# Kernel tuning notes

Hardware: AMD Instinct MI355X
Metric: run time of the kernel (lower is better)

The kernel has to match this reference:

```python
import jax, jax.numpy as jnp
import numpy as np

NU = 160000   # users
NM = 60000    # movies
D = 64        # embedding dim
E = 5000000   # rating edges
L = 200000    # label edges to score
NUM_LAYERS = 3


def setup_inputs() -> dict:
    key = jax.random.key(0)
    k1, k2, k3, k4, k5, k6 = jax.random.split(key, 6)
    return {
        "emb_user": jax.random.normal(k1, (NU, D), jnp.float32),
        "emb_movie": jax.random.normal(k2, (NM, D), jnp.float32),
        "node_id_user": jnp.arange(NU),
        "node_id_movie": jnp.arange(NM),
        "edge_from": jax.random.randint(k3, (E,), 0, NM),   # movie side of each edge
        "edge_to": jax.random.randint(k4, (E,), 0, NU),     # user side of each edge
        "label_movie": jax.random.randint(k5, (L,), 0, NM),
        "label_user": jax.random.randint(k6, (L,), 0, NU),
    }


def reference(emb_user, emb_movie, node_id_user, node_id_movie,
              edge_from, edge_to, label_movie, label_user):
    # Embedding lookup (node_id is an arange over all nodes in the batch)
    x_u = emb_user[node_id_user]    # [NU, D]
    x_m = emb_movie[node_id_movie]  # [NM, D]

    # Symmetric degree normalization: deg(from)^-1/2 * deg(to)^-1/2 per edge
    ones = jnp.ones(edge_from.shape[0], dtype=x_m.dtype)
    deg_m = jax.ops.segment_sum(ones, edge_from, num_segments=NM)
    deg_u = jax.ops.segment_sum(ones, edge_to, num_segments=NU)
    inv_m = jnp.where(deg_m > 0, deg_m ** -0.5, 0.0)
    inv_u = jnp.where(deg_u > 0, deg_u ** -0.5, 0.0)
    norm = inv_m[edge_from] * inv_u[edge_to]  # [E]

    # NOTE: the original torch code never writes the propagated embeddings back
    # into x_dict, so every layer propagates the layer-0 embeddings. Replicated
    # faithfully here.
    embs_u = [x_u]
    embs_m = [x_m]
    for _ in range(NUM_LAYERS):
        # movie -> user aggregation (x2y): gather movie feats, scale, scatter-add to users
        u_agg = jax.ops.segment_sum(norm[:, None] * x_m[edge_from], edge_to, num_segments=NU)
        m_agg = jax.ops.segment_sum(norm[:, None] * x_u[edge_to], edge_from, num_segments=NM)
        embs_u.append(u_agg)
        embs_m.append(m_agg)

    # Layer combination with weights 1/(l+1)
    w = 1.0 / (jnp.arange(NUM_LAYERS + 1, dtype=x_u.dtype) + 1.0)
    res_u = jnp.einsum('l,lnd->nd', w, jnp.stack(embs_u))  # [NU, D]
    res_m = jnp.einsum('l,lnd->nd', w, jnp.stack(embs_m))  # [NM, D]

    # Classifier: dot product over label edges
    scores = jnp.sum(res_u[label_user] * res_m[label_movie], axis=-1)  # [L]
    return (scores, res_u, res_m)
```

## Files before the change

kernel.cpp:

```cpp
#include <hip/hip_runtime.h>
#include <hip/hip_bf16.h>

#define NU 160000
#define NM 60000
#define DD 64
#define NE 5000000
#define NL 200000

#define COEF (13.0f / 12.0f)

#define SHIFT_U 9
#define SHIFT_M 7
#define NBU ((NU + (1 << SHIFT_U) - 1) >> SHIFT_U)
#define NBM ((NM + (1 << SHIFT_M) - 1) >> SHIFT_M)
#define VB_U 16
#define VB_M 18

#define UDIV 30000
#define LG_U 1
#define MDIV 20000
#define BS 1024
#define NVU2 (NBU << 10)
#define NVM2 (NBM << 10)


#define CEC 16

__global__ void bucket_count_kernel(const int* __restrict__ ef, const int* __restrict__ et,
                                    int* __restrict__ gbh_u, int* __restrict__ gbh_m) {
    __shared__ int bhu[NBU], bhm[NBM];
    int tid = threadIdx.x;
    for (int i = tid; i < NBU; i += 256) bhu[i] = 0;
    for (int i = tid; i < NBM; i += 256) bhm[i] = 0;
    __syncthreads();
    int base = (blockIdx.x * 256 + tid) * CEC;
    if (base < NE) {
        const int4* f4 = (const int4*)(ef + base);
        const int4* t4 = (const int4*)(et + base);
        #pragma unroll
        for (int q = 0; q < CEC / 4; q++) {
            int4 ff = f4[q]; int4 tt = t4[q];
            atomicAdd(&bhm[ff.x >> SHIFT_M], 1); atomicAdd(&bhu[tt.x >> SHIFT_U], 1);
            atomicAdd(&bhm[ff.y >> SHIFT_M], 1); atomicAdd(&bhu[tt.y >> SHIFT_U], 1);
            atomicAdd(&bhm[ff.z >> SHIFT_M], 1); atomicAdd(&bhu[tt.z >> SHIFT_U], 1);
            atomicAdd(&bhm[ff.w >> SHIFT_M], 1); atomicAdd(&bhu[tt.w >> SHIFT_U], 1);
        }
    }
    __syncthreads();
    for (int i = tid; i < NBU; i += 256) if (bhu[i]) atomicAdd(&gbh_u[i], bhu[i]);
    for (int i = tid; i < NBM; i += 256) if (bhm[i]) atomicAdd(&gbh_m[i], bhm[i]);
}


__global__ void scan_small_kernel(const int* __restrict__ in, int* __restrict__ out,
                                  int* __restrict__ cur, int n) {
    __shared__ int buf[256];
    int tid = threadIdx.x;
    int idx = tid * 4;
    int v0 = (idx + 0 < n) ? in[idx + 0] : 0;
    int v1 = (idx + 1 < n) ? in[idx + 1] : 0;
    int v2 = (idx + 2 < n) ? in[idx + 2] : 0;
    int v3 = (idx + 3 < n) ? in[idx + 3] : 0;
    int s = v0 + v1 + v2 + v3;
    buf[tid] = s;
    __syncthreads();
    for (int off = 1; off < 256; off <<= 1) {
        int t = (tid >= off) ? buf[tid - off] : 0;
        __syncthreads();
        buf[tid] += t;
        __syncthreads();
    }
    int p = buf[tid] - s;
    if (idx + 0 < n) { out[idx + 0] = p; if (cur) cur[idx + 0] = p; p += v0; }
    if (idx + 1 < n) { out[idx + 1] = p; if (cur) cur[idx + 1] = p; p += v1; }
    if (idx + 2 < n) { out[idx + 2] = p; if (cur) cur[idx + 2] = p; p += v2; }
    if (idx + 3 < n) { out[idx + 3] = p; if (cur) cur[idx + 3] = p; p += v3; }
    if (tid == 255) out[n] = buf[255];
}


#define PEC 16

__global__ void partition_kernel(const int* __restrict__ key, const int* __restrict__ val,
                                 int* __restrict__ bcur, int* __restrict__ stage,
                                 int nb, int shift, int valbits, int mode) {
    __shared__ int lh[512];
    __shared__ int lbase[512];
    int tid = threadIdx.x;
    for (int i = tid; i < nb; i += 256) lh[i] = 0;
    __syncthreads();
    int base = (blockIdx.x * 256 + tid) * PEC;
    int lk_[PEC], v_[PEC], br_[PEC];
    bool act = base < NE;
    if (act) {
        int k_[PEC];
        const int4* k4 = (const int4*)(key + base);
        const int4* v4 = (const int4*)(val + base);
        #pragma unroll
        for (int q = 0; q < PEC / 4; q++) {
            int4 kk = k4[q]; int4 vv = v4[q];
            k_[q * 4 + 0] = kk.x; k_[q * 4 + 1] = kk.y; k_[q * 4 + 2] = kk.z; k_[q * 4 + 3] = kk.w;
            v_[q * 4 + 0] = vv.x; v_[q * 4 + 1] = vv.y; v_[q * 4 + 2] = vv.z; v_[q * 4 + 3] = vv.w;
        }
        #pragma unroll
        for (int q = 0; q < PEC; q++) {
            int k = k_[q];
            int lk;
            if (mode == 0) lk = ((k & 511) << 1) | (v_[q] >= UDIV ? 1 : 0);
            else           lk = ((int)((unsigned)v_[q] / MDIV) << 7) | (k & 127);
            lk_[q] = lk;
            int b = k >> shift;
            int r = atomicAdd(&lh[b], 1);
            br_[q] = (b << 13) | r;
        }
    }
    __syncthreads();
    for (int i = tid; i < nb; i += 256) lbase[i] = lh[i] ? atomicAdd(&bcur[i], lh[i]) : 0;
    __syncthreads();
    if (act) {
        #pragma unroll
        for (int q = 0; q < PEC; q++) {
            int b = br_[q] >> 13;
            int r = br_[q] & 8191;
            stage[lbase[b] + r] = (lk_[q] << valbits) | v_[q];
        }
    }
}


__global__ void build_kernel(const int* __restrict__ stage, const int* __restrict__ bo,
                             int* __restrict__ rp, int* __restrict__ pay,
                             int n, int valbits, int pmask) {
    __shared__ int cnt[BS];
    __shared__ int tmp[BS];
    int b = blockIdx.x;
    int tid = threadIdx.x;
    int base = b << 10;
    int nn = min(BS, n - base);
    int vmask = (1 << valbits) - 1;
    int s0 = bo[b];
    int s1 = bo[b + 1];

    for (int i = tid; i < BS; i += 256) cnt[i] = 0;
    __syncthreads();
    for (int e = s0 + tid; e < s1; e += 256)
        atomicAdd(&cnt[stage[e] >> valbits], 1);
    __syncthreads();
    int ov[4];
    #pragma unroll
    for (int q = 0; q < 4; q++) ov[q] = cnt[tid + q * 256];
    for (int off = 1; off < BS; off <<= 1) {
        int t[4];
        #pragma unroll
        for (int q = 0; q < 4; q++) {
            int i = tid + q * 256;
            t[q] = (i >= off) ? cnt[i - off] : 0;
        }
        __syncthreads();
        #pragma unroll
        for (int q = 0; q < 4; q++) cnt[tid + q * 256] += t[q];
        __syncthreads();
    }
    #pragma unroll
    for (int q = 0; q < 4; q++) {
        int i = tid + q * 256;
        int excl = cnt[i] - ov[q];
        tmp[i] = s0 + excl;
        if (i < nn) rp[base + i] = s0 + excl;
    }
    if (b == 0 && tid == 0) rp[n] = NE;
    __syncthreads();
    for (int e = s0 + tid; e < s1; e += 256) {
        int p = stage[e];
        int k = p >> valbits;
        int pos = atomicAdd(&tmp[k], 1);
        pay[pos] = (p & vmask) | ((k & pmask) << valbits);
    }
}


__global__ void inv_from_rp_kernel(const int* __restrict__ rp, float* __restrict__ inv,
                                   int n, int lg) {
    int i = blockIdx.x * blockDim.x + threadIdx.x;
    if (i < n) {
        int d = rp[(i + 1) << lg] - rp[i << lg];
        inv[i] = (d > 0) ? rsqrtf((float)d) : 0.0f;
    }
}

__global__ void inv_m_from_rp_kernel(const int* __restrict__ rp, float* __restrict__ inv) {
    int f = blockIdx.x * blockDim.x + threadIdx.x;
    if (f < NM) {
        int base = ((f >> 7) << 10) | (f & 127);
        int d = 0;
        #pragma unroll
        for (int h = 0; h < 8; h++) {
            int idx = base + (h << 7);
            d += rp[idx + 1] - rp[idx];
        }
        inv[f] = (d > 0) ? rsqrtf((float)d) : 0.0f;
    }
}


__global__ void prescale_kernel(const float* __restrict__ x, const float* __restrict__ inv,
                                __hip_bfloat16* __restrict__ y, int total) {
    int i = blockIdx.x * blockDim.x + threadIdx.x;
    if (i < total) {
        int node = i >> 6;
        y[i] = __float2bfloat16(inv[node] * x[i]);
    }
}


__global__ void gather_u_kernel(const int* __restrict__ rp, const int* __restrict__ pay,
                                const float* __restrict__ inv_dst,
                                const __hip_bfloat16* __restrict__ y_src,
                                const float* __restrict__ x_dst,
                                float* __restrict__ res, int n) {
    int tid = blockIdx.x * blockDim.x + threadIdx.x;
    int node = tid >> 6;
    int lane = threadIdx.x & 63;
    if (node >= n) return;
    int start = rp[node << LG_U];
    int end   = rp[(node + 1) << LG_U];
    float acc = 0.0f;
    for (int i = start; i < end; i += 64) {
        int cnt = min(end - i, 64);
        int nid = (lane < cnt) ? pay[i + lane] : 0;
        int j = 0;
        for (; j + 4 <= cnt; j += 4) {
            int f0 = __shfl(nid, j + 0, 64);
            int f1 = __shfl(nid, j + 1, 64);
            int f2 = __shfl(nid, j + 2, 64);
            int f3 = __shfl(nid, j + 3, 64);
            float a0 = __bfloat162float(y_src[f0 * DD + lane]);
            float a1 = __bfloat162float(y_src[f1 * DD + lane]);
            float a2 = __bfloat162float(y_src[f2 * DD + lane]);
            float a3 = __bfloat162float(y_src[f3 * DD + lane]);
            acc += a0 + a1 + a2 + a3;
        }
        for (; j < cnt; j++) {
            int f0 = __shfl(nid, j, 64);
            acc += __bfloat162float(y_src[f0 * DD + lane]);
        }
    }
    int o = node * DD + lane;
    res[o] = x_dst[o] + COEF * inv_dst[node] * acc;
}


__global__ __launch_bounds__(1024) void gather_m_kernel(
        const int* __restrict__ rp, const int* __restrict__ pay,
        const float* __restrict__ inv_dst,
        const __hip_bfloat16* __restrict__ y_src,
        const float* __restrict__ x_dst,
        float* __restrict__ res) {
    __shared__ float acc[128 * DD];
    int b = blockIdx.x;
    int tid = threadIdx.x;
    int wave = tid >> 6;
    int lane = tid & 63;
    for (int i = tid; i < 128 * DD; i += 1024) acc[i] = 0.0f;
    __syncthreads();

    int vbase = b << 10;
    const int umask = (1 << VB_M) - 1;
    float racc = 0.0f;
    int rm = -1;
    for (int h = 0; h < 8; h++) {
        int s0 = rp[vbase + (h << 7)];
        int s1 = rp[vbase + (h << 7) + 128];
        int total = s1 - s0;
        if (total <= 0) continue;
        int per = (total + 15) >> 4;
        int e0 = s0 + wave * per;
        int e1 = min(e0 + per, s1);
        for (int i = e0; i < e1; i += 64) {
            int cnt = min(e1 - i, 64);
            int pv = (lane < cnt) ? pay[i + lane] : 0;
            int j = 0;
            for (; j + 4 <= cnt; j += 4) {
                int p0 = __shfl(pv, j + 0, 64);
                int p1 = __shfl(pv, j + 1, 64);
                int p2 = __shfl(pv, j + 2, 64);
                int p3 = __shfl(pv, j + 3, 64);
                float a0 = __bfloat162float(y_src[(p0 & umask) * DD + lane]);
                float a1 = __bfloat162float(y_src[(p1 & umask) * DD + lane]);
                float a2 = __bfloat162float(y_src[(p2 & umask) * DD + lane]);
                float a3 = __bfloat162float(y_src[(p3 & umask) * DD + lane]);
                int m0 = p0 >> VB_M;
                if (m0 != rm) { if (rm >= 0) atomicAdd(&acc[rm * DD + lane], racc); rm = m0; racc = a0; }
                else racc += a0;
                int m1 = p1 >> VB_M;
                if (m1 != rm) { if (rm >= 0) atomicAdd(&acc[rm * DD + lane], racc); rm = m1; racc = a1; }
                else racc += a1;
                int m2 = p2 >> VB_M;
                if (m2 != rm) { if (rm >= 0) atomicAdd(&acc[rm * DD + lane], racc); rm = m2; racc = a2; }
                else racc += a2;
                int m3 = p3 >> VB_M;
                if (m3 != rm) { if (rm >= 0) atomicAdd(&acc[rm * DD + lane], racc); rm = m3; racc = a3; }
                else racc += a3;
            }
            for (; j < cnt; j++) {
                int p0 = __shfl(pv, j, 64);
                float a0 = __bfloat162float(y_src[(p0 & umask) * DD + lane]);
                int m0 = p0 >> VB_M;
                if (m0 != rm) { if (rm >= 0) atomicAdd(&acc[rm * DD + lane], racc); rm = m0; racc = a0; }
                else racc += a0;
            }
        }
    }
    if (rm >= 0) atomicAdd(&acc[rm * DD + lane], racc);
    __syncthreads();

    int nn = min(128, NM - (b << 7));
    int lim = nn * DD;
    int gbase = (b << 7) * DD;
    for (int i = tid; i < lim; i += 1024) {
        int f = (b << 7) + (i >> 6);
        res[gbase + i] = x_dst[gbase + i] + COEF * inv_dst[f] * acc[i];
    }
}


__global__ void score_kernel(const int* __restrict__ lm, const int* __restrict__ lu,
                             const float* __restrict__ ru, const float* __restrict__ rm,
                             float* __restrict__ scores) {
    int tid = blockIdx.x * blockDim.x + threadIdx.x;
    int l = tid >> 6;
    int d = threadIdx.x & 63;
    if (l < NL) {
        int u = lu[l];
        int m = lm[l];
        float v = ru[u * DD + d] * rm[m * DD + d];
        #pragma unroll
        for (int off = 32; off >= 1; off >>= 1)
            v += __shfl_down(v, off, 64);
        if (d == 0) scores[l] = v;
    }
}


__global__ void degree_kernel_f(const int* __restrict__ ef, const int* __restrict__ et,
                                float* __restrict__ deg_m, float* __restrict__ deg_u) {
    int i = blockIdx.x * blockDim.x + threadIdx.x;
    if (i < NE) {
        atomicAdd(&deg_m[ef[i]], 1.0f);
        atomicAdd(&deg_u[et[i]], 1.0f);
    }
}

__global__ void inv_kernel_f(float* __restrict__ deg, int n) {
    int i = blockIdx.x * blockDim.x + threadIdx.x;
    if (i < n) {
        float d = deg[i];
        deg[i] = (d > 0.0f) ? (1.0f / sqrtf(d)) : 0.0f;
    }
}

__global__ void agg_kernel_f(const int* __restrict__ ef, const int* __restrict__ et,
                             const float* __restrict__ inv_m, const float* __restrict__ inv_u,
                             const float* __restrict__ x_u, const float* __restrict__ x_m,
                             float* __restrict__ res_u, float* __restrict__ res_m) {
    int tid = blockIdx.x * blockDim.x + threadIdx.x;
    int e = tid >> 6;
    int d = tid & 63;
    if (e < NE) {
        int f = ef[e];
        int t = et[e];
        float norm = inv_m[f] * inv_u[t] * COEF;
        atomicAdd(&res_u[t * DD + d], norm * x_m[f * DD + d]);
        atomicAdd(&res_m[f * DD + d], norm * x_u[t * DD + d]);
    }
}

__global__ void add_base_kernel_f(const float* __restrict__ xu, const float* __restrict__ xm,
                                  float* __restrict__ ru, float* __restrict__ rm) {
    int i = blockIdx.x * blockDim.x + threadIdx.x;
    const int nu = NU * DD;
    const int nm = NM * DD;
    if (i < nu) {
        ru[i] += xu[i];
    } else if (i < nu + nm) {
        int j = i - nu;
        rm[j] += xm[j];
    }
}


extern "C" void kernel_launch(void* const* d_in, const int* in_sizes, int n_in,
                              void* d_out, int out_size, void* d_ws, size_t ws_size,
                              hipStream_t stream) {
    const float* emb_user  = (const float*)d_in[0];
    const float* emb_movie = (const float*)d_in[1];
    const int* edge_from   = (const int*)d_in[4];
    const int* edge_to     = (const int*)d_in[5];
    const int* label_movie = (const int*)d_in[6];
    const int* label_user  = (const int*)d_in[7];

    float* out    = (float*)d_out;
    float* scores = out;
    float* res_u  = out + NL;
    float* res_m  = out + NL + (size_t)NU * DD;

    int*   gbh_u  = (int*)d_ws;
    int*   gbh_m  = gbh_u + NBU;
    int*   bo_u   = gbh_m + NBM;
    int*   bcur_u = bo_u + NBU + 1;
    int*   bo_m   = bcur_u + NBU;
    int*   bcur_m = bo_m + NBM + 1;
    float* inv_u  = (float*)(bcur_m + NBM);
    float* inv_m  = inv_u + NU;
    int*   rp_u   = (int*)(inv_m + NM);
    int*   rp_m   = rp_u + NVU2 + 1;
    int*   pay_u  = rp_m + NVM2 + 1;
    int*   pay_m  = pay_u + NE;
    int*   ureg   = pay_m + NE;
    int*   stage  = ureg;
    __hip_bfloat16* y_u = (__hip_bfloat16*)ureg;
    __hip_bfloat16* y_m = (__hip_bfloat16*)(ureg + (size_t)NU * DD / 2);

    size_t ysz    = (size_t)(NU + NM) * DD / 2;
    size_t uni    = (size_t)NE > ysz ? (size_t)NE : ysz;
    size_t needed = ((size_t)(ureg - (int*)d_ws) + uni) * sizeof(int);

    if (ws_size >= needed) {
        hipMemsetAsync(gbh_u, 0, (size_t)(NBU + NBM) * sizeof(int), stream);

        bucket_count_kernel<<<(NE / CEC + 255) / 256, 256, 0, stream>>>(
            edge_from, edge_to, gbh_u, gbh_m);
        scan_small_kernel<<<1, 256, 0, stream>>>(gbh_u, bo_u, bcur_u, NBU);
        scan_small_kernel<<<1, 256, 0, stream>>>(gbh_m, bo_m, bcur_m, NBM);

        partition_kernel<<<(NE / PEC + 255) / 256, 256, 0, stream>>>(
            edge_to, edge_from, bcur_u, stage, NBU, SHIFT_U, VB_U, 0);
        build_kernel<<<NBU, 256, 0, stream>>>(stage, bo_u, rp_u, pay_u, NVU2, VB_U, 0);

        partition_kernel<<<(NE / PEC + 255) / 256, 256, 0, stream>>>(
            edge_from, edge_to, bcur_m, stage, NBM, SHIFT_M, VB_M, 1);
        build_kernel<<<NBM, 256, 0, stream>>>(stage, bo_m, rp_m, pay_m, NVM2, VB_M, 127);

        inv_from_rp_kernel<<<(NU + 255) / 256, 256, 0, stream>>>(rp_u, inv_u, NU, LG_U);
        inv_m_from_rp_kernel<<<(NM + 255) / 256, 256, 0, stream>>>(rp_m, inv_m);

        prescale_kernel<<<((size_t)NU * DD + 255) / 256, 256, 0, stream>>>(
            emb_user, inv_u, y_u, NU * DD);
        prescale_kernel<<<((size_t)NM * DD + 255) / 256, 256, 0, stream>>>(
            emb_movie, inv_m, y_m, NM * DD);

        gather_u_kernel<<<((size_t)NU * 64 + 255) / 256, 256, 0, stream>>>(
            rp_u, pay_u, inv_u, y_m, emb_user, res_u, NU);
        gather_m_kernel<<<NBM, 1024, 0, stream>>>(
            rp_m, pay_m, inv_m, y_u, emb_movie, res_m);
    } else {
        float* fdeg_u = (float*)d_ws;
        float* fdeg_m = fdeg_u + NU;
        hipMemsetAsync(res_u, 0, (size_t)(NU + NM) * DD * sizeof(float), stream);
        hipMemsetAsync(fdeg_u, 0, (size_t)(NU + NM) * sizeof(float), stream);
        degree_kernel_f<<<(NE + 255) / 256, 256, 0, stream>>>(edge_from, edge_to, fdeg_m, fdeg_u);
        inv_kernel_f<<<(NU + NM + 255) / 256, 256, 0, stream>>>(fdeg_u, NU + NM);
        agg_kernel_f<<<((size_t)NE * 64 + 255) / 256, 256, 0, stream>>>(
            edge_from, edge_to, fdeg_m, fdeg_u, emb_user, emb_movie, res_u, res_m);
        add_base_kernel_f<<<((NU + NM) * DD + 255) / 256, 256, 0, stream>>>(
            emb_user, emb_movie, res_u, res_m);
    }

    score_kernel<<<((size_t)NL * 64 + 255) / 256, 256, 0, stream>>>(
        label_movie, label_user, res_u, res_m, scores);
}
```

Measured before the change: 867.4 us.

## Shrink movie buckets to 64 nodes with 13 user phases and direct LDS atomics

Movie-side buckets drop from 128 to 64 nodes, and the user dimension is split into 13 phases instead of 8, so the partition key and the degree lookup change to match. The movie gather runs with 512 threads and a smaller shared accumulator. It drops the run-length merging of consecutive same-movie contributions and instead does an unrolled atomicAdd per edge, using a sentinel row to absorb padding lanes. The user gather unrolls to 8 loads per step for more memory-level parallelism. The trade-off is more LDS atomics and more blocks in exchange for higher occupancy and fewer branches.

```diff
diff --git a/kernel.cpp b/kernel.cpp
--- a/kernel.cpp
+++ b/kernel.cpp
@@ -10,7 +10,7 @@
 #define COEF (13.0f / 12.0f)
 
 #define SHIFT_U 9
-#define SHIFT_M 7
+#define SHIFT_M 6
 #define NBU ((NU + (1 << SHIFT_U) - 1) >> SHIFT_U)
 #define NBM ((NM + (1 << SHIFT_M) - 1) >> SHIFT_M)
 #define VB_U 16
@@ -18,7 +18,8 @@
 
 #define UDIV 30000
 #define LG_U 1
-#define MDIV 20000
+#define MDIV 13000
+#define NPH_M 13
 #define BS 1024
 #define NVU2 (NBU << 10)
 #define NVM2 (NBM << 10)
@@ -84,8 +85,8 @@
 __global__ void partition_kernel(const int* __restrict__ key, const int* __restrict__ val,
                                  int* __restrict__ bcur, int* __restrict__ stage,
                                  int nb, int shift, int valbits, int mode) {
-    __shared__ int lh[512];
-    __shared__ int lbase[512];
+    __shared__ int lh[1024];
+    __shared__ int lbase[1024];
     int tid = threadIdx.x;
     for (int i = tid; i < nb; i += 256) lh[i] = 0;
     __syncthreads();
@@ -107,7 +108,7 @@
             int k = k_[q];
             int lk;
             if (mode == 0) lk = ((k & 511) << 1) | (v_[q] >= UDIV ? 1 : 0);
-            else           lk = ((int)((unsigned)v_[q] / MDIV) << 7) | (k & 127);
+            else           lk = ((int)((unsigned)v_[q] / MDIV) << 6) | (k & 63);
             lk_[q] = lk;
             int b = k >> shift;
             int r = atomicAdd(&lh[b], 1);
@@ -191,11 +192,11 @@
 __global__ void inv_m_from_rp_kernel(const int* __restrict__ rp, float* __restrict__ inv) {
     int f = blockIdx.x * blockDim.x + threadIdx.x;
     if (f < NM) {
-        int base = ((f >> 7) << 10) | (f & 127);
+        int base = ((f >> 6) << 10) | (f & 63);
         int d = 0;
         #pragma unroll
-        for (int h = 0; h < 8; h++) {
-            int idx = base + (h << 7);
+        for (int h = 0; h < NPH_M; h++) {
+            int idx = base + (h << 6);
             d += rp[idx + 1] - rp[idx];
         }
         inv[f] = (d > 0) ? rsqrtf((float)d) : 0.0f;
@@ -229,16 +230,16 @@
         int cnt = min(end - i, 64);
         int nid = (lane < cnt) ? pay[i + lane] : 0;
         int j = 0;
-        for (; j + 4 <= cnt; j += 4) {
-            int f0 = __shfl(nid, j + 0, 64);
-            int f1 = __shfl(nid, j + 1, 64);
-            int f2 = __shfl(nid, j + 2, 64);
-            int f3 = __shfl(nid, j + 3, 64);
-            float a0 = __bfloat162float(y_src[f0 * DD + lane]);
-            float a1 = __bfloat162float(y_src[f1 * DD + lane]);
-            float a2 = __bfloat162float(y_src[f2 * DD + lane]);
-            float a3 = __bfloat162float(y_src[f3 * DD + lane]);
-            acc += a0 + a1 + a2 + a3;
+        for (; j + 8 <= cnt; j += 8) {
+            float a0 = __bfloat162float(y_src[__shfl(nid, j + 0, 64) * DD + lane]);
+            float a1 = __bfloat162float(y_src[__shfl(nid, j + 1, 64) * DD + lane]);
+            float a2 = __bfloat162float(y_src[__shfl(nid, j + 2, 64) * DD + lane]);
+            float a3 = __bfloat162float(y_src[__shfl(nid, j + 3, 64) * DD + lane]);
+            float a4 = __bfloat162float(y_src[__shfl(nid, j + 4, 64) * DD + lane]);
+            float a5 = __bfloat162float(y_src[__shfl(nid, j + 5, 64) * DD + lane]);
+            float a6 = __bfloat162float(y_src[__shfl(nid, j + 6, 64) * DD + lane]);
+            float a7 = __bfloat162float(y_src[__shfl(nid, j + 7, 64) * DD + lane]);
+            acc += ((a0 + a1) + (a2 + a3)) + ((a4 + a5) + (a6 + a7));
         }
         for (; j < cnt; j++) {
             int f0 = __shfl(nid, j, 64);
@@ -250,75 +251,51 @@
 }
 
 
-__global__ __launch_bounds__(1024) void gather_m_kernel(
+__global__ __launch_bounds__(512) void gather_m_kernel(
         const int* __restrict__ rp, const int* __restrict__ pay,
         const float* __restrict__ inv_dst,
         const __hip_bfloat16* __restrict__ y_src,
         const float* __restrict__ x_dst,
         float* __restrict__ res) {
-    __shared__ float acc[128 * DD];
+    __shared__ float acc[65 * DD];
     int b = blockIdx.x;
     int tid = threadIdx.x;
     int wave = tid >> 6;
     int lane = tid & 63;
-    for (int i = tid; i < 128 * DD; i += 1024) acc[i] = 0.0f;
+    for (int i = tid; i < 65 * DD; i += 512) acc[i] = 0.0f;
     __syncthreads();
 
     int vbase = b << 10;
     const int umask = (1 << VB_M) - 1;
-    float racc = 0.0f;
-    int rm = -1;
-    for (int h = 0; h < 8; h++) {
-        int s0 = rp[vbase + (h << 7)];
-        int s1 = rp[vbase + (h << 7) + 128];
+    const int SENT = 64 << VB_M;
+    for (int h = 0; h < NPH_M; h++) {
+        int s0 = rp[vbase + (h << 6)];
+        int s1 = rp[vbase + (h << 6) + 64];
         int total = s1 - s0;
-        if (total <= 0) continue;
-        int per = (total + 15) >> 4;
+        int per = (total + 7) >> 3;
         int e0 = s0 + wave * per;
         int e1 = min(e0 + per, s1);
         for (int i = e0; i < e1; i += 64) {
             int cnt = min(e1 - i, 64);
-            int pv = (lane < cnt) ? pay[i + lane] : 0;
-            int j = 0;
-            for (; j + 4 <= cnt; j += 4) {
-                int p0 = __shfl(pv, j + 0, 64);
-                int p1 = __shfl(pv, j + 1, 64);
-                int p2 = __shfl(pv, j + 2, 64);
-                int p3 = __shfl(pv, j + 3, 64);
-                float a0 = __bfloat162float(y_src[(p0 & umask) * DD + lane]);
-                float a1 = __bfloat162float(y_src[(p1 & umask) * DD + lane]);
-                float a2 = __bfloat162float(y_src[(p2 & umask) * DD + lane]);
-                float a3 = __bfloat162float(y_src[(p3 & umask) * DD + lane]);
-                int m0 = p0 >> VB_M;
-                if (m0 != rm) { if (rm >= 0) atomicAdd(&acc[rm * DD + lane], racc); rm = m0; racc = a0; }
-                else racc += a0;
-                int m1 = p1 >> VB_M;
-                if (m1 != rm) { if (rm >= 0) atomicAdd(&acc[rm * DD + lane], racc); rm = m1; racc = a1; }
-                else racc += a1;
-                int m2 = p2 >> VB_M;
-                if (m2 != rm) { if (rm >= 0) atomicAdd(&acc[rm * DD + lane], racc); rm = m2; racc = a2; }
-                else racc += a2;
-                int m3 = p3 >> VB_M;
-                if (m3 != rm) { if (rm >= 0) atomicAdd(&acc[rm * DD + lane], racc); rm = m3; racc = a3; }
-                else racc += a3;
+            int pv = (lane < cnt) ? pay[i + lane] : SENT;
+            int jmax = (cnt + 15) & ~15;
+            for (int j = 0; j < jmax; j += 16) {
+                #pragma unroll
+                for (int k = 0; k < 16; k++) {
+                    int p = __shfl(pv, j + k, 64);
+                    float a = __bfloat162float(y_src[(p & umask) * DD + lane]);
+                    atomicAdd(&acc[(p >> VB_M) * DD + lane], a);
+                }
             }
-            for (; j < cnt; j++) {
-                int p0 = __shfl(pv, j, 64);
-                float a0 = __bfloat162float(y_src[(p0 & umask) * DD + lane]);
-                int m0 = p0 >> VB_M;
-                if (m0 != rm) { if (rm >= 0) atomicAdd(&acc[rm * DD + lane], racc); rm = m0; racc = a0; }
-                else racc += a0;
-            }
-        }
-    }
-    if (rm >= 0) atomicAdd(&acc[rm * DD + lane], racc);
-    __syncthreads();
-
-    int nn = min(128, NM - (b << 7));
-    int lim = nn * DD;
-    int gbase = (b << 7) * DD;
-    for (int i = tid; i < lim; i += 1024) {
-        int f = (b << 7) + (i >> 6);
+        }
+        __syncthreads();
+    }
+
+    int mb = b << 6;
+    int nn = min(64, NM - mb);
+    int gbase = mb * DD;
+    for (int i = tid; i < nn * DD; i += 512) {
+        int f = mb + (i >> 6);
         res[gbase + i] = x_dst[gbase + i] + COEF * inv_dst[f] * acc[i];
     }
 }
@@ -439,7 +416,7 @@
 
         partition_kernel<<<(NE / PEC + 255) / 256, 256, 0, stream>>>(
             edge_from, edge_to, bcur_m, stage, NBM, SHIFT_M, VB_M, 1);
-        build_kernel<<<NBM, 256, 0, stream>>>(stage, bo_m, rp_m, pay_m, NVM2, VB_M, 127);
+        build_kernel<<<NBM, 256, 0, stream>>>(stage, bo_m, rp_m, pay_m, NVM2, VB_M, 63);
 
         inv_from_rp_kernel<<<(NU + 255) / 256, 256, 0, stream>>>(rp_u, inv_u, NU, LG_U);
         inv_m_from_rp_kernel<<<(NM + 255) / 256, 256, 0, stream>>>(rp_m, inv_m);
@@ -451,7 +428,7 @@
 
         gather_u_kernel<<<((size_t)NU * 64 + 255) / 256, 256, 0, stream>>>(
             rp_u, pay_u, inv_u, y_m, emb_user, res_u, NU);
-        gather_m_kernel<<<NBM, 1024, 0, stream>>>(
+        gather_m_kernel<<<NBM, 512, 0, stream>>>(
             rp_m, pay_m, inv_m, y_u, emb_movie, res_m);
     } else {
         float* fdeg_u = (float*)d_ws;
```

Measured after the change: 2.721 ms. +213.7%, slower.
